# Performance work log

Hardware: AMD Instinct MI355X
Metric: run time of the kernel (lower is better)

The kernel has to match this reference:

```python
import jax, jax.numpy as jnp
import numpy as np

N = 50000
E = 800000
F_IN = 128
HID = 128
NCLS = 64


def setup_inputs() -> dict:
    key = jax.random.key(0)
    ks = jax.random.split(key, 10)
    x = jax.random.normal(ks[0], (N, F_IN), dtype=jnp.float32)
    edge_index = jax.random.randint(ks[1], (2, E), 0, N, dtype=jnp.int64)
    def w(k, fi, fo):
        return jax.random.normal(k, (fi, fo), dtype=jnp.float32) / np.sqrt(fi)
    return {
        "x": x,
        "edge_index": edge_index,
        "W1": w(ks[2], F_IN, HID), "b1": jnp.zeros((HID,), jnp.float32),
        "W2": w(ks[3], HID, HID), "b2": jnp.zeros((HID,), jnp.float32),
        "W3": w(ks[4], HID, HID), "b3": jnp.zeros((HID,), jnp.float32),
        "W4": w(ks[5], HID, NCLS), "b4": jnp.zeros((NCLS,), jnp.float32),
    }


def _build_graph(edge_index, n):
    # PyG GCNConv default: add self loops, symmetric normalization D^-1/2 (A+I) D^-1/2
    loops = jnp.arange(n, dtype=edge_index.dtype)
    row = jnp.concatenate([edge_index[0], loops])  # source
    col = jnp.concatenate([edge_index[1], loops])  # destination
    deg = jax.ops.segment_sum(jnp.ones_like(col, dtype=jnp.float32), col, num_segments=n)
    dinv = jnp.where(deg > 0, jax.lax.rsqrt(deg), 0.0)
    norm = dinv[row] * dinv[col]  # [E+N]
    return row, col, norm


def _gcn_layer(x, row, col, norm, W, b, n):
    h = x @ W                                    # [N, out]
    msg = h[row] * norm[:, None]                 # gather + scale, [E+N, out]
    out = jax.ops.segment_sum(msg, col, num_segments=n)  # scatter-add
    return out + b


def reference(x, edge_index, W1, b1, W2, b2, W3, b3, W4, b4):
    n = x.shape[0]
    row, col, norm = _build_graph(edge_index, n)
    h = jax.nn.relu(_gcn_layer(x, row, col, norm, W1, b1, n))
    h = jax.nn.relu(_gcn_layer(h, row, col, norm, W2, b2, n))
    h = jax.nn.relu(_gcn_layer(h, row, col, norm, W3, b3, n))
    return _gcn_layer(h, row, col, norm, W4, b4, n)
```

## Files before the change

### kernel.cpp

```cpp
#include <hip/hip_runtime.h>
#include <hip/hip_fp16.h>
#include <type_traits>

#define N_NODES 50000
#define N_EDGES 800000
#define WIN_BITS 9
#define WIN 512
#define NBUK ((N_NODES + WIN - 1) / WIN)
#define BCAP 16384

typedef _Float16 half8 __attribute__((ext_vector_type(8)));
typedef float floatx4 __attribute__((ext_vector_type(4)));

__device__ inline void acc8(float* a, half8 v) {
    const __half2* p = (const __half2*)&v;
    float2 f0 = __half22float2(p[0]);
    float2 f1 = __half22float2(p[1]);
    float2 f2 = __half22float2(p[2]);
    float2 f3 = __half22float2(p[3]);
    a[0] += f0.x; a[1] += f0.y; a[2] += f1.x; a[3] += f1.y;
    a[4] += f2.x; a[5] += f2.y; a[6] += f3.x; a[7] += f3.y;
}

__global__ __launch_bounds__(256) void p0_bucket(const int* __restrict__ ei,
                                                 int* __restrict__ gcur,
                                                 unsigned* __restrict__ arena, int E) {
    __shared__ int lcnt[NBUK];
    __shared__ int lbase[NBUK];
    int tid = threadIdx.x;
    int chunk = (E + gridDim.x - 1) / gridDim.x;
    int e0 = blockIdx.x * chunk;
    int e1 = e0 + chunk; if (e1 > E) e1 = E;
    for (int b = tid; b < NBUK; b += 256) lcnt[b] = 0;
    __syncthreads();
    for (int e = e0 + tid; e < e1; e += 256) {
        int dst = ei[E + e];
        atomicAdd(&lcnt[dst >> WIN_BITS], 1);
    }
    __syncthreads();
    for (int b = tid; b < NBUK; b += 256) {
        lbase[b] = atomicAdd(&gcur[b], lcnt[b]);
        lcnt[b] = 0;
    }
    __syncthreads();
    for (int e = e0 + tid; e < e1; e += 256) {
        int dst = ei[E + e];
        int src = ei[e];
        int b = dst >> WIN_BITS;
        int pos = lbase[b] + atomicAdd(&lcnt[b], 1);
        if (pos < BCAP)
            arena[(size_t)b * BCAP + pos] = ((unsigned)src << WIN_BITS) | (unsigned)(dst & (WIN - 1));
    }
}

__global__ void scan_buckets(const int* __restrict__ gcur, int* __restrict__ bukoff,
                             int* __restrict__ offsets, int n, int total) {
    __shared__ int s[128];
    int t = threadIdx.x;
    int v = (t < NBUK) ? gcur[t] : 0;
    s[t] = v;
    __syncthreads();
    for (int off = 1; off < 128; off <<= 1) {
        int u = (t >= off) ? s[t - off] : 0;
        __syncthreads();
        s[t] += u;
        __syncthreads();
    }
    if (t < NBUK) bukoff[t] = s[t] - v;
    if (t == 0) offsets[n] = total;
}

__global__ __launch_bounds__(256) void p1_count_scan(const unsigned* __restrict__ arena,
                                                     const int* __restrict__ gcur,
                                                     const int* __restrict__ bukoff,
                                                     int* __restrict__ offsets,
                                                     float* __restrict__ dinv, int n) {
    __shared__ int cnt[WIN];
    __shared__ int sbuf[256];
    int b = blockIdx.x, tid = threadIdx.x;
    cnt[tid] = 0; cnt[tid + 256] = 0;
    __syncthreads();
    int m = gcur[b]; if (m > BCAP) m = BCAP;
    const unsigned* a = arena + (size_t)b * BCAP;
    for (int i = tid; i < m; i += 256) atomicAdd(&cnt[a[i] & (WIN - 1)], 1);
    __syncthreads();
    int j0 = tid * 2;
    int a0 = cnt[j0], a1 = cnt[j0 + 1];
    int ts = a0 + a1;
    sbuf[tid] = ts;
    __syncthreads();
    for (int off = 1; off < 256; off <<= 1) {
        int u = (tid >= off) ? sbuf[tid - off] : 0;
        __syncthreads();
        sbuf[tid] += u;
        __syncthreads();
    }
    int pre = sbuf[tid] - ts;
    int base = b << WIN_BITS;
    int o0 = bukoff[b] + pre, o1 = o0 + a0;
    int d0 = base + j0;
    if (d0 + 1 < n) {
        *(int2*)&offsets[d0] = make_int2(o0, o1);
        *(float2*)&dinv[d0] = make_float2(rsqrtf((float)(a0 + 1)), rsqrtf((float)(a1 + 1)));
    } else if (d0 < n) {
        offsets[d0] = o0;
        dinv[d0] = rsqrtf((float)(a0 + 1));
    }
}

__global__ __launch_bounds__(256) void p2_fill(const unsigned* __restrict__ arena,
                                               const int* __restrict__ gcur,
                                               const int* __restrict__ offsets,
                                               int* __restrict__ csr_src, int n) {
    __shared__ int cur[WIN];
    int b = blockIdx.x, tid = threadIdx.x;
    int base = b << WIN_BITS;
    for (int j = tid; j < WIN; j += 256) {
        int d = base + j;
        cur[j] = (d < n) ? offsets[d] : 0;
    }
    __syncthreads();
    int m = gcur[b]; if (m > BCAP) m = BCAP;
    const unsigned* a = arena + (size_t)b * BCAP;
    for (int i = tid; i < m; i += 256) {
        unsigned e = a[i];
        int pos = atomicAdd(&cur[e & (WIN - 1)], 1);
        csr_src[pos] = (int)(e >> WIN_BITS);
    }
}

__global__ __launch_bounds__(256) void wfrag_all(
        const float* __restrict__ W1, const float* __restrict__ W2,
        const float* __restrict__ W3, const float* __restrict__ W4,
        _Float16* __restrict__ Wf1, _Float16* __restrict__ Wf2,
        _Float16* __restrict__ Wf3, _Float16* __restrict__ Wf4) {
    int b = blockIdx.x;
    const float* W; _Float16* Wf; int FO; int lb;
    if (b < 8)       { W = W1; Wf = Wf1; FO = 128; lb = b; }
    else if (b < 16) { W = W2; Wf = Wf2; FO = 128; lb = b - 8; }
    else if (b < 24) { W = W3; Wf = Wf3; FO = 128; lb = b - 16; }
    else             { W = W4; Wf = Wf4; FO = 64;  lb = b - 24; }
    int g = lb * 256 + threadIdx.x;
    if (g >= 16 * FO) return;
    int col = g % FO;
    int sq = g / FO;
    int k0 = sq * 8;
    half8 hv;
    #pragma unroll
    for (int j = 0; j < 8; ++j)
        hv[j] = (_Float16)W[(size_t)(k0 + j) * FO + col];
    *(half8*)&Wf[(size_t)g * 8] = hv;
}

__global__ __launch_bounds__(256) void gemm_mfma_kernel(
        const float* __restrict__ x, const _Float16* __restrict__ Wfrag,
        const float* __restrict__ dinv, __half* __restrict__ h, int n) {
    constexpr int FO = 128;
    constexpr int NT = FO / 16;
    int tid = threadIdx.x;
    int ln = tid & 15;
    int q  = (tid >> 4) & 3;
    int w  = tid >> 6;
    int node = blockIdx.x * 64 + w * 16 + ln;
    int nodec = node < n ? node : n - 1;
    const float* xrow = x + (size_t)nodec * 128;

    floatx4 acc[NT];
    #pragma unroll
    for (int t = 0; t < NT; ++t) acc[t] = (floatx4){0.f, 0.f, 0.f, 0.f};

    #pragma unroll
    for (int s = 0; s < 4; ++s) {
        const float* xp = xrow + s * 32 + q * 8;
        float4 a0 = *(const float4*)xp;
        float4 a1 = *(const float4*)(xp + 4);
        half8 xf;
        xf[0] = (_Float16)a0.x; xf[1] = (_Float16)a0.y;
        xf[2] = (_Float16)a0.z; xf[3] = (_Float16)a0.w;
        xf[4] = (_Float16)a1.x; xf[5] = (_Float16)a1.y;
        xf[6] = (_Float16)a1.z; xf[7] = (_Float16)a1.w;
        int sq = s * 4 + q;
        #pragma unroll
        for (int t = 0; t < NT; ++t) {
            half8 wf = *(const half8*)&Wfrag[(size_t)(sq * FO + t * 16 + ln) * 8];
            acc[t] = __builtin_amdgcn_mfma_f32_16x16x32_f16(wf, xf, acc[t], 0, 0, 0);
        }
    }

    if (node < n) {
        float dv = dinv[node];
        __half* hrow = h + (size_t)node * FO;
        #pragma unroll
        for (int t = 0; t < NT; ++t) {
            __half2 p[2];
            p[0] = __float22half2_rn(make_float2(acc[t][0] * dv, acc[t][1] * dv));
            p[1] = __float22half2_rn(make_float2(acc[t][2] * dv, acc[t][3] * dv));
            *(uint2*)&hrow[t * 16 + q * 4] = *(const uint2*)p;
        }
    }
}

template<int FO>
__global__ __launch_bounds__(512) void fused_agg_gemm(
        const _Float16* __restrict__ hin, const int* __restrict__ offsets,
        const int* __restrict__ csr_src, const float* __restrict__ dinv,
        const float* __restrict__ bias, const _Float16* __restrict__ Wfrag,
        __half* __restrict__ hout, int n) {
    constexpr int NT  = FO / 16;
    constexpr int TPW = NT / 2;
    __shared__ _Float16 aggL[64 * 136];

    int tid = threadIdx.x;
    int w = tid >> 6;
    int lane = tid & 63;
    int qw = lane >> 4, sl = lane & 15;
    float4 bb0 = *(const float4*)&bias[sl * 8];
    float4 bb1 = *(const float4*)&bias[sl * 8 + 4];

    for (int ii = 0; ii < 8; ++ii) {
        int c = blockIdx.x * 64 + w * 8 + ii;
        if (c >= n) break;
        c = __builtin_amdgcn_readfirstlane(c);
        float acc[8] = {0.f, 0.f, 0.f, 0.f, 0.f, 0.f, 0.f, 0.f};
        if (qw == 0)
            acc8(acc, *(const half8*)&hin[(size_t)c * 128 + sl * 8]);
        int s = offsets[c], e = offsets[c + 1];
        int i = s;
        for (; i + 7 < e; i += 8) {
            int sa = csr_src[i + qw];
            int sb = csr_src[i + 4 + qw];
            half8 va = *(const half8*)&hin[(size_t)sa * 128 + sl * 8];
            half8 vb = *(const half8*)&hin[(size_t)sb * 128 + sl * 8];
            acc8(acc, va);
            acc8(acc, vb);
        }
        for (; i + 3 < e; i += 4) {
            int sa = csr_src[i + qw];
            acc8(acc, *(const half8*)&hin[(size_t)sa * 128 + sl * 8]);
        }
        if (i + qw < e) {
            int sa = csr_src[i + qw];
            acc8(acc, *(const half8*)&hin[(size_t)sa * 128 + sl * 8]);
        }
        #pragma unroll
        for (int k = 0; k < 8; ++k) {
            acc[k] += __shfl_xor(acc[k], 16);
            acc[k] += __shfl_xor(acc[k], 32);
        }
        if (qw == 0) {
            float dc = dinv[c];
            float v0 = fmaxf(fmaf(acc[0], dc, bb0.x), 0.f);
            float v1 = fmaxf(fmaf(acc[1], dc, bb0.y), 0.f);
            float v2 = fmaxf(fmaf(acc[2], dc, bb0.z), 0.f);
            float v3 = fmaxf(fmaf(acc[3], dc, bb0.w), 0.f);
            float v4 = fmaxf(fmaf(acc[4], dc, bb1.x), 0.f);
            float v5 = fmaxf(fmaf(acc[5], dc, bb1.y), 0.f);
            float v6 = fmaxf(fmaf(acc[6], dc, bb1.z), 0.f);
            float v7 = fmaxf(fmaf(acc[7], dc, bb1.w), 0.f);
            half8 hv;
            hv[0] = (_Float16)v0; hv[1] = (_Float16)v1;
            hv[2] = (_Float16)v2; hv[3] = (_Float16)v3;
            hv[4] = (_Float16)v4; hv[5] = (_Float16)v5;
            hv[6] = (_Float16)v6; hv[7] = (_Float16)v7;
            *(half8*)&aggL[(size_t)(w * 8 + ii) * 136 + sl * 8] = hv;
        }
    }
    __syncthreads();

    int ng = w & 3, cg = w >> 2;
    int ln = tid & 15;
    int q  = (tid >> 4) & 3;
    int nl = ng * 16 + ln;
    int node = blockIdx.x * 64 + nl;

    floatx4 acc[TPW];
    #pragma unroll
    for (int t = 0; t < TPW; ++t) acc[t] = (floatx4){0.f, 0.f, 0.f, 0.f};

    #pragma unroll
    for (int s = 0; s < 4; ++s) {
        half8 xf = *(const half8*)&aggL[(size_t)nl * 136 + s * 32 + q * 8];
        int sq = s * 4 + q;
        #pragma unroll
        for (int t = 0; t < TPW; ++t) {
            int T = cg * TPW + t;
            half8 wf = *(const half8*)&Wfrag[(size_t)(sq * FO + T * 16 + ln) * 8];
            acc[t] = __builtin_amdgcn_mfma_f32_16x16x32_f16(wf, xf, acc[t], 0, 0, 0);
        }
    }

    if (node < n) {
        float dv = dinv[node];
        __half* hrow = hout + (size_t)node * FO;
        #pragma unroll
        for (int t = 0; t < TPW; ++t) {
            int T = cg * TPW + t;
            __half2 p[2];
            p[0] = __float22half2_rn(make_float2(acc[t][0] * dv, acc[t][1] * dv));
            p[1] = __float22half2_rn(make_float2(acc[t][2] * dv, acc[t][3] * dv));
            *(uint2*)&hrow[T * 16 + q * 4] = *(const uint2*)p;
        }
    }
}

__global__ __launch_bounds__(256) void agg64_kernel(
        const _Float16* __restrict__ h, const int* __restrict__ offsets,
        const int* __restrict__ csr_src, const float* __restrict__ dinv,
        const float* __restrict__ bias, float* __restrict__ out, int n) {
    int lane = threadIdx.x & 63;
    int o = lane >> 3, sl = lane & 7;
    int c = (blockIdx.x << 2) + (threadIdx.x >> 6);
    if (c >= n) return;
    c = __builtin_amdgcn_readfirstlane(c);
    float acc[8] = {0.f, 0.f, 0.f, 0.f, 0.f, 0.f, 0.f, 0.f};
    if (o == 0)
        acc8(acc, *(const half8*)&h[(size_t)c * 64 + sl * 8]);
    int s = offsets[c], e = offsets[c + 1];
    int i = s;
    for (; i + 15 < e; i += 16) {
        int sa = csr_src[i + o];
        int sb = csr_src[i + 8 + o];
        half8 va = *(const half8*)&h[(size_t)sa * 64 + sl * 8];
        half8 vb = *(const half8*)&h[(size_t)sb * 64 + sl * 8];
        acc8(acc, va);
        acc8(acc, vb);
    }
    for (; i + 7 < e; i += 8) {
        int sa = csr_src[i + o];
        acc8(acc, *(const half8*)&h[(size_t)sa * 64 + sl * 8]);
    }
    if (i + o < e) {
        int sa = csr_src[i + o];
        acc8(acc, *(const half8*)&h[(size_t)sa * 64 + sl * 8]);
    }
    #pragma unroll
    for (int k = 0; k < 8; ++k) {
        acc[k] += __shfl_xor(acc[k], 8);
        acc[k] += __shfl_xor(acc[k], 16);
        acc[k] += __shfl_xor(acc[k], 32);
    }
    if (o == 0) {
        float dc = dinv[c];
        float4 bb0 = *(const float4*)&bias[sl * 8];
        float4 bb1 = *(const float4*)&bias[sl * 8 + 4];
        float4 o0, o1;
        o0.x = fmaf(acc[0], dc, bb0.x); o0.y = fmaf(acc[1], dc, bb0.y);
        o0.z = fmaf(acc[2], dc, bb0.z); o0.w = fmaf(acc[3], dc, bb0.w);
        o1.x = fmaf(acc[4], dc, bb1.x); o1.y = fmaf(acc[5], dc, bb1.y);
        o1.z = fmaf(acc[6], dc, bb1.z); o1.w = fmaf(acc[7], dc, bb1.w);
        float* orow = out + (size_t)c * 64 + sl * 8;
        *(float4*)orow = o0;
        *(float4*)(orow + 4) = o1;
    }
}


extern "C" void kernel_launch(void* const* d_in, const int* in_sizes, int n_in,
                              void* d_out, int out_size, void* d_ws, size_t ws_size,
                              hipStream_t stream) {
    const float* x  = (const float*)d_in[0];
    const int*   ei = (const int*)  d_in[1];
    const float* W1 = (const float*)d_in[2];
    const float* b1 = (const float*)d_in[3];
    const float* W2 = (const float*)d_in[4];
    const float* b2 = (const float*)d_in[5];
    const float* W3 = (const float*)d_in[6];
    const float* b3 = (const float*)d_in[7];
    const float* W4 = (const float*)d_in[8];
    const float* b4 = (const float*)d_in[9];

    const int N = N_NODES, E = N_EDGES;

    char* p = (char*)d_ws;
    auto carve = [&](size_t bytes) {
        char* q = p;
        p += (bytes + 255) & ~(size_t)255;
        return (void*)q;
    };
    int*       offsets = (int*)      carve((size_t)(N + 1) * 4);
    int*       csr_src = (int*)      carve((size_t)E * 4);
    float*     dinv    = (float*)    carve((size_t)N * 4);
    int*       gcur    = (int*)      carve((size_t)NBUK * 4);
    int*       bukoff  = (int*)      carve((size_t)NBUK * 4);
    unsigned*  arena   = (unsigned*) carve((size_t)NBUK * BCAP * 4);
    _Float16*  Wf1     = (_Float16*) carve((size_t)16 * 128 * 8 * 2);
    _Float16*  Wf2     = (_Float16*) carve((size_t)16 * 128 * 8 * 2);
    _Float16*  Wf3     = (_Float16*) carve((size_t)16 * 128 * 8 * 2);
    _Float16*  Wf4     = (_Float16*) carve((size_t)16 * 64 * 8 * 2);
    __half*    A1      = (__half*)   carve((size_t)N * 128 * 2);
    __half*    A2      = (__half*)   carve((size_t)N * 128 * 2);

    hipMemsetAsync(gcur, 0, (size_t)NBUK * 4, stream);
    p0_bucket<<<512, 256, 0, stream>>>(ei, gcur, arena, E);
    scan_buckets<<<1, 128, 0, stream>>>(gcur, bukoff, offsets, N, E);
    p1_count_scan<<<NBUK, 256, 0, stream>>>(arena, gcur, bukoff, offsets, dinv, N);
    p2_fill<<<NBUK, 256, 0, stream>>>(arena, gcur, offsets, csr_src, N);
    wfrag_all<<<28, 256, 0, stream>>>(W1, W2, W3, W4, Wf1, Wf2, Wf3, Wf4);

    const int nb64 = (N + 63) / 64;

    gemm_mfma_kernel<<<nb64, 256, 0, stream>>>(x, Wf1, dinv, A1, N);
    fused_agg_gemm<128><<<nb64, 512, 0, stream>>>((const _Float16*)A1, offsets, csr_src, dinv, b1, Wf2, A2, N);
    fused_agg_gemm<128><<<nb64, 512, 0, stream>>>((const _Float16*)A2, offsets, csr_src, dinv, b2, Wf3, A1, N);
    fused_agg_gemm<64><<<nb64, 512, 0, stream>>>((const _Float16*)A1, offsets, csr_src, dinv, b3, Wf4, A2, N);
    agg64_kernel<<<(N + 3) / 4, 256, 0, stream>>>((const _Float16*)A2, offsets, csr_src, dinv, b4, (float*)d_out, N);
}
```

Before: 280.8 us.

## Fuse graph-build kernels and interleave two destination nodes in aggregation

Folds the weight-fragment conversion into the edge-bucketing kernel and merges the bucket scan, count/scan and CSR fill into one build_graph kernel. Each block now recomputes its bucket offset with a shared-memory reduction. This cuts the preprocessing launches from five to two. The fused aggregation loop now walks two destination nodes at once, so two independent gather streams are in flight per wave, which raises memory-level parallelism at the cost of more registers and extra tail loops.

```diff
diff --git a/kernel.cpp b/kernel.cpp
--- a/kernel.cpp
+++ b/kernel.cpp
@@ -22,13 +22,36 @@
     a[4] += f2.x; a[5] += f2.y; a[6] += f3.x; a[7] += f3.y;
 }
 
-__global__ __launch_bounds__(256) void p0_bucket(const int* __restrict__ ei,
-                                                 int* __restrict__ gcur,
-                                                 unsigned* __restrict__ arena, int E) {
+__global__ __launch_bounds__(256) void p0_wfrag(
+        const int* __restrict__ ei, int* __restrict__ gcur,
+        unsigned* __restrict__ arena, int E,
+        const float* __restrict__ W1, const float* __restrict__ W2,
+        const float* __restrict__ W3, const float* __restrict__ W4,
+        _Float16* __restrict__ Wf1, _Float16* __restrict__ Wf2,
+        _Float16* __restrict__ Wf3, _Float16* __restrict__ Wf4) {
+    int tid = threadIdx.x;
+    if (blockIdx.x >= 512) {
+        int b = blockIdx.x - 512;
+        const float* W; _Float16* Wf; int FO; int lb;
+        if (b < 8)       { W = W1; Wf = Wf1; FO = 128; lb = b; }
+        else if (b < 16) { W = W2; Wf = Wf2; FO = 128; lb = b - 8; }
+        else if (b < 24) { W = W3; Wf = Wf3; FO = 128; lb = b - 16; }
+        else             { W = W4; Wf = Wf4; FO = 64;  lb = b - 24; }
+        int g = lb * 256 + tid;
+        if (g >= 16 * FO) return;
+        int col = g % FO;
+        int sq = g / FO;
+        int k0 = sq * 8;
+        half8 hv;
+        #pragma unroll
+        for (int j = 0; j < 8; ++j)
+            hv[j] = (_Float16)W[(size_t)(k0 + j) * FO + col];
+        *(half8*)&Wf[(size_t)g * 8] = hv;
+        return;
+    }
     __shared__ int lcnt[NBUK];
     __shared__ int lbase[NBUK];
-    int tid = threadIdx.x;
-    int chunk = (E + gridDim.x - 1) / gridDim.x;
+    int chunk = (E + 511) / 512;
     int e0 = blockIdx.x * chunk;
     int e1 = e0 + chunk; if (e1 > E) e1 = E;
     for (int b = tid; b < NBUK; b += 256) lcnt[b] = 0;
@@ -53,37 +76,30 @@
     }
 }
 
-__global__ void scan_buckets(const int* __restrict__ gcur, int* __restrict__ bukoff,
-                             int* __restrict__ offsets, int n, int total) {
-    __shared__ int s[128];
-    int t = threadIdx.x;
-    int v = (t < NBUK) ? gcur[t] : 0;
-    s[t] = v;
-    __syncthreads();
-    for (int off = 1; off < 128; off <<= 1) {
-        int u = (t >= off) ? s[t - off] : 0;
-        __syncthreads();
-        s[t] += u;
-        __syncthreads();
-    }
-    if (t < NBUK) bukoff[t] = s[t] - v;
-    if (t == 0) offsets[n] = total;
-}
-
-__global__ __launch_bounds__(256) void p1_count_scan(const unsigned* __restrict__ arena,
-                                                     const int* __restrict__ gcur,
-                                                     const int* __restrict__ bukoff,
-                                                     int* __restrict__ offsets,
-                                                     float* __restrict__ dinv, int n) {
+__global__ __launch_bounds__(256) void build_graph(
+        const unsigned* __restrict__ arena, const int* __restrict__ gcur,
+        int* __restrict__ offsets, float* __restrict__ dinv,
+        int* __restrict__ csr_src, int n, int total) {
     __shared__ int cnt[WIN];
     __shared__ int sbuf[256];
+    __shared__ int bukoff_s;
     int b = blockIdx.x, tid = threadIdx.x;
+
+    sbuf[tid] = (tid < b) ? gcur[tid] : 0;
     cnt[tid] = 0; cnt[tid + 256] = 0;
     __syncthreads();
+    #pragma unroll
+    for (int off = 128; off > 0; off >>= 1) {
+        if (tid < off) sbuf[tid] += sbuf[tid + off];
+        __syncthreads();
+    }
+    if (tid == 0) bukoff_s = sbuf[0];
+
     int m = gcur[b]; if (m > BCAP) m = BCAP;
     const unsigned* a = arena + (size_t)b * BCAP;
     for (int i = tid; i < m; i += 256) atomicAdd(&cnt[a[i] & (WIN - 1)], 1);
     __syncthreads();
+
     int j0 = tid * 2;
     int a0 = cnt[j0], a1 = cnt[j0 + 1];
     int ts = a0 + a1;
@@ -97,7 +113,7 @@
     }
     int pre = sbuf[tid] - ts;
     int base = b << WIN_BITS;
-    int o0 = bukoff[b] + pre, o1 = o0 + a0;
+    int o0 = bukoff_s + pre, o1 = o0 + a0;
     int d0 = base + j0;
     if (d0 + 1 < n) {
         *(int2*)&offsets[d0] = make_int2(o0, o1);
@@ -106,50 +122,15 @@
         offsets[d0] = o0;
         dinv[d0] = rsqrtf((float)(a0 + 1));
     }
-}
-
-__global__ __launch_bounds__(256) void p2_fill(const unsigned* __restrict__ arena,
-                                               const int* __restrict__ gcur,
-                                               const int* __restrict__ offsets,
-                                               int* __restrict__ csr_src, int n) {
-    __shared__ int cur[WIN];
-    int b = blockIdx.x, tid = threadIdx.x;
-    int base = b << WIN_BITS;
-    for (int j = tid; j < WIN; j += 256) {
-        int d = base + j;
-        cur[j] = (d < n) ? offsets[d] : 0;
-    }
-    __syncthreads();
-    int m = gcur[b]; if (m > BCAP) m = BCAP;
-    const unsigned* a = arena + (size_t)b * BCAP;
+    __syncthreads();
+    cnt[j0] = o0; cnt[j0 + 1] = o1;
+    __syncthreads();
     for (int i = tid; i < m; i += 256) {
         unsigned e = a[i];
-        int pos = atomicAdd(&cur[e & (WIN - 1)], 1);
+        int pos = atomicAdd(&cnt[e & (WIN - 1)], 1);
         csr_src[pos] = (int)(e >> WIN_BITS);
     }
-}
-
-__global__ __launch_bounds__(256) void wfrag_all(
-        const float* __restrict__ W1, const float* __restrict__ W2,
-        const float* __restrict__ W3, const float* __restrict__ W4,
-        _Float16* __restrict__ Wf1, _Float16* __restrict__ Wf2,
-        _Float16* __restrict__ Wf3, _Float16* __restrict__ Wf4) {
-    int b = blockIdx.x;
-    const float* W; _Float16* Wf; int FO; int lb;
-    if (b < 8)       { W = W1; Wf = Wf1; FO = 128; lb = b; }
-    else if (b < 16) { W = W2; Wf = Wf2; FO = 128; lb = b - 8; }
-    else if (b < 24) { W = W3; Wf = Wf3; FO = 128; lb = b - 16; }
-    else             { W = W4; Wf = Wf4; FO = 64;  lb = b - 24; }
-    int g = lb * 256 + threadIdx.x;
-    if (g >= 16 * FO) return;
-    int col = g % FO;
-    int sq = g / FO;
-    int k0 = sq * 8;
-    half8 hv;
-    #pragma unroll
-    for (int j = 0; j < 8; ++j)
-        hv[j] = (_Float16)W[(size_t)(k0 + j) * FO + col];
-    *(half8*)&Wf[(size_t)g * 8] = hv;
+    if (b == 0 && tid == 0) offsets[n] = total;
 }
 
 __global__ __launch_bounds__(256) void gemm_mfma_kernel(
@@ -217,52 +198,82 @@
     float4 bb0 = *(const float4*)&bias[sl * 8];
     float4 bb1 = *(const float4*)&bias[sl * 8 + 4];
 
-    for (int ii = 0; ii < 8; ++ii) {
-        int c = blockIdx.x * 64 + w * 8 + ii;
-        if (c >= n) break;
-        c = __builtin_amdgcn_readfirstlane(c);
-        float acc[8] = {0.f, 0.f, 0.f, 0.f, 0.f, 0.f, 0.f, 0.f};
-        if (qw == 0)
-            acc8(acc, *(const half8*)&hin[(size_t)c * 128 + sl * 8]);
-        int s = offsets[c], e = offsets[c + 1];
-        int i = s;
-        for (; i + 7 < e; i += 8) {
-            int sa = csr_src[i + qw];
-            int sb = csr_src[i + 4 + qw];
+    for (int pp = 0; pp < 4; ++pp) {
+        int c0 = blockIdx.x * 64 + w * 8 + pp * 2;
+        if (c0 >= n) break;
+        int c1 = c0 + 1;
+        bool v1 = c1 < n;
+        c0 = __builtin_amdgcn_readfirstlane(c0);
+        c1 = __builtin_amdgcn_readfirstlane(c1);
+
+        float a0[8] = {0.f, 0.f, 0.f, 0.f, 0.f, 0.f, 0.f, 0.f};
+        float a1[8] = {0.f, 0.f, 0.f, 0.f, 0.f, 0.f, 0.f, 0.f};
+        if (qw == 0) acc8(a0, *(const half8*)&hin[(size_t)c0 * 128 + sl * 8]);
+        if (v1 && qw == 0) acc8(a1, *(const half8*)&hin[(size_t)c1 * 128 + sl * 8]);
+
+        int i0 = offsets[c0], e0 = offsets[c0 + 1];
+        int i1 = v1 ? offsets[c1] : 0, e1 = v1 ? offsets[c1 + 1] : 0;
+
+        while (i0 + 3 < e0 && i1 + 3 < e1) {
+            int sa = csr_src[i0 + qw];
+            int sb = csr_src[i1 + qw];
             half8 va = *(const half8*)&hin[(size_t)sa * 128 + sl * 8];
             half8 vb = *(const half8*)&hin[(size_t)sb * 128 + sl * 8];
-            acc8(acc, va);
-            acc8(acc, vb);
-        }
-        for (; i + 3 < e; i += 4) {
-            int sa = csr_src[i + qw];
-            acc8(acc, *(const half8*)&hin[(size_t)sa * 128 + sl * 8]);
-        }
-        if (i + qw < e) {
-            int sa = csr_src[i + qw];
-            acc8(acc, *(const half8*)&hin[(size_t)sa * 128 + sl * 8]);
-        }
+            acc8(a0, va);
+            acc8(a1, vb);
+            i0 += 4; i1 += 4;
+        }
+        for (; i0 + 3 < e0; i0 += 4) {
+            int sa = csr_src[i0 + qw];
+            acc8(a0, *(const half8*)&hin[(size_t)sa * 128 + sl * 8]);
+        }
+        if (i0 + qw < e0) {
+            int sa = csr_src[i0 + qw];
+            acc8(a0, *(const half8*)&hin[(size_t)sa * 128 + sl * 8]);
+        }
+        for (; i1 + 3 < e1; i1 += 4) {
+            int sb = csr_src[i1 + qw];
+            acc8(a1, *(const half8*)&hin[(size_t)sb * 128 + sl * 8]);
+        }
+        if (v1 && i1 + qw < e1) {
+            int sb = csr_src[i1 + qw];
+            acc8(a1, *(const half8*)&hin[(size_t)sb * 128 + sl * 8]);
+        }
+
         #pragma unroll
         for (int k = 0; k < 8; ++k) {
-            acc[k] += __shfl_xor(acc[k], 16);
-            acc[k] += __shfl_xor(acc[k], 32);
+            a0[k] += __shfl_xor(a0[k], 16);
+            a0[k] += __shfl_xor(a0[k], 32);
+            a1[k] += __shfl_xor(a1[k], 16);
+            a1[k] += __shfl_xor(a1[k], 32);
         }
         if (qw == 0) {
-            float dc = dinv[c];
-            float v0 = fmaxf(fmaf(acc[0], dc, bb0.x), 0.f);
-            float v1 = fmaxf(fmaf(acc[1], dc, bb0.y), 0.f);
-            float v2 = fmaxf(fmaf(acc[2], dc, bb0.z), 0.f);
-            float v3 = fmaxf(fmaf(acc[3], dc, bb0.w), 0.f);
-            float v4 = fmaxf(fmaf(acc[4], dc, bb1.x), 0.f);
-            float v5 = fmaxf(fmaf(acc[5], dc, bb1.y), 0.f);
-            float v6 = fmaxf(fmaf(acc[6], dc, bb1.z), 0.f);
-            float v7 = fmaxf(fmaf(acc[7], dc, bb1.w), 0.f);
-            half8 hv;
-            hv[0] = (_Float16)v0; hv[1] = (_Float16)v1;
-            hv[2] = (_Float16)v2; hv[3] = (_Float16)v3;
-            hv[4] = (_Float16)v4; hv[5] = (_Float16)v5;
-            hv[6] = (_Float16)v6; hv[7] = (_Float16)v7;
-            *(half8*)&aggL[(size_t)(w * 8 + ii) * 136 + sl * 8] = hv;
+            {
+                float dc = dinv[c0];
+                half8 hv;
+                hv[0] = (_Float16)fmaxf(fmaf(a0[0], dc, bb0.x), 0.f);
+                hv[1] = (_Float16)fmaxf(fmaf(a0[1], dc, bb0.y), 0.f);
+                hv[2] = (_Float16)fmaxf(fmaf(a0[2], dc, bb0.z), 0.f);
+                hv[3] = (_Float16)fmaxf(fmaf(a0[3], dc, bb0.w), 0.f);
+                hv[4] = (_Float16)fmaxf(fmaf(a0[4], dc, bb1.x), 0.f);
+                hv[5] = (_Float16)fmaxf(fmaf(a0[5], dc, bb1.y), 0.f);
+                hv[6] = (_Float16)fmaxf(fmaf(a0[6], dc, bb1.z), 0.f);
+                hv[7] = (_Float16)fmaxf(fmaf(a0[7], dc, bb1.w), 0.f);
+                *(half8*)&aggL[(size_t)(w * 8 + pp * 2) * 136 + sl * 8] = hv;
+            }
+            if (v1) {
+                float dc = dinv[c1];
+                half8 hv;
+                hv[0] = (_Float16)fmaxf(fmaf(a1[0], dc, bb0.x), 0.f);
+                hv[1] = (_Float16)fmaxf(fmaf(a1[1], dc, bb0.y), 0.f);
+                hv[2] = (_Float16)fmaxf(fmaf(a1[2], dc, bb0.z), 0.f);
+                hv[3] = (_Float16)fmaxf(fmaf(a1[3], dc, bb0.w), 0.f);
+                hv[4] = (_Float16)fmaxf(fmaf(a1[4], dc, bb1.x), 0.f);
+                hv[5] = (_Float16)fmaxf(fmaf(a1[5], dc, bb1.y), 0.f);
+                hv[6] = (_Float16)fmaxf(fmaf(a1[6], dc, bb1.z), 0.f);
+                hv[7] = (_Float16)fmaxf(fmaf(a1[7], dc, bb1.w), 0.f);
+                *(half8*)&aggL[(size_t)(w * 8 + pp * 2 + 1) * 136 + sl * 8] = hv;
+            }
         }
     }
     __syncthreads();
@@ -381,7 +392,6 @@
     int*       csr_src = (int*)      carve((size_t)E * 4);
     float*     dinv    = (float*)    carve((size_t)N * 4);
     int*       gcur    = (int*)      carve((size_t)NBUK * 4);
-    int*       bukoff  = (int*)      carve((size_t)NBUK * 4);
     unsigned*  arena   = (unsigned*) carve((size_t)NBUK * BCAP * 4);
     _Float16*  Wf1     = (_Float16*) carve((size_t)16 * 128 * 8 * 2);
     _Float16*  Wf2     = (_Float16*) carve((size_t)16 * 128 * 8 * 2);
@@ -391,11 +401,9 @@
     __half*    A2      = (__half*)   carve((size_t)N * 128 * 2);
 
     hipMemsetAsync(gcur, 0, (size_t)NBUK * 4, stream);
-    p0_bucket<<<512, 256, 0, stream>>>(ei, gcur, arena, E);
-    scan_buckets<<<1, 128, 0, stream>>>(gcur, bukoff, offsets, N, E);
-    p1_count_scan<<<NBUK, 256, 0, stream>>>(arena, gcur, bukoff, offsets, dinv, N);
-    p2_fill<<<NBUK, 256, 0, stream>>>(arena, gcur, offsets, csr_src, N);
-    wfrag_all<<<28, 256, 0, stream>>>(W1, W2, W3, W4, Wf1, Wf2, Wf3, Wf4);
+    p0_wfrag<<<540, 256, 0, stream>>>(ei, gcur, arena, E,
+                                      W1, W2, W3, W4, Wf1, Wf2, Wf3, Wf4);
+    build_graph<<<NBUK, 256, 0, stream>>>(arena, gcur, offsets, dinv, csr_src, N, E);
 
     const int nb64 = (N + 63) / 64;
 
```

Result: no change. 277.0 us (-1.3%).
